# Kernel tuning notes

Hardware: AMD Instinct MI355X
Metric: run time of the kernel (lower is better)

The kernel has to match this reference:

```python
import jax, jax.numpy as jnp
import numpy as np

N, CIO, L = 16, 512, 384
DIMHEAD, NUMHEAD, MAXEMBED, DIMGROUP = 64, 8, 384, 8
CHID = DIMHEAD * NUMHEAD


def setup_inputs() -> dict:
    key = jax.random.key(0)
    ks = jax.random.split(key, 12)
    s = 0.05
    return {
        "x": jax.random.normal(ks[0], (N, CIO, L), jnp.float32),
        "xorg": jax.random.normal(ks[1], (N, CIO, L), jnp.float32),
        "abspos": jax.random.normal(ks[2], (N, CIO, L), jnp.float32),
        "mask": jnp.zeros((N, L), jnp.float32),
        "norm": jnp.full((N,), 8.0, jnp.float32),
        "qkpos_res": s * jax.random.normal(ks[3], (CIO // DIMGROUP, 1), jnp.float32),
        "qkorg_res": s * jax.random.normal(ks[4], (CIO // DIMGROUP, 1), jnp.float32),
        "vorg_res": s * jax.random.normal(ks[5], (CIO // DIMGROUP, 1), jnp.float32),
        "relpos": s * jax.random.normal(ks[6], (2 * MAXEMBED - 1,), jnp.float32),
        "gate_w": s * jax.random.normal(ks[7], (NUMHEAD, CIO), jnp.float32),
        "gate_b": jnp.zeros((NUMHEAD,), jnp.float32),
        "q_w": s * jax.random.normal(ks[8], (CHID, CIO), jnp.float32),
        "k_w": s * jax.random.normal(ks[9], (CHID, CIO), jnp.float32),
        "v_w": s * jax.random.normal(ks[10], (CHID, CIO), jnp.float32),
        "dense_w": s * jax.random.normal(ks[11], (CIO, CHID), jnp.float32),
        "dense_b": jnp.zeros((CIO,), jnp.float32),
    }


def _rezero(t, res):
    # (N,C,L) -> reshape to (N, C//DIMGROUP, DIMGROUP*L), scale per group, reshape back
    n, c, l = t.shape
    return (t.reshape(n, c // DIMGROUP, -1) * res).reshape(n, c, l)


def _relpos_idx():
    # idx[i, j] = clip(MAXEMBED - i + j, 0, 2*MAXEMBED - 2)
    idx = np.arange(MAXEMBED, MAXEMBED - L, -1)[:, None] + np.arange(L)[None, :]
    return jnp.asarray(np.clip(idx, 0, 2 * MAXEMBED - 2))


def reference(x, xorg, abspos, mask, norm, qkpos_res, qkorg_res, vorg_res,
              relpos, gate_w, gate_b, q_w, k_w, v_w, dense_w, dense_b):
    n = x.shape[0]
    x0 = x + _rezero(xorg, vorg_res)                     # value path
    x1 = x + _rezero(xorg, qkorg_res) + _rezero(abspos, qkpos_res)  # qk path

    q = jnp.einsum('oc,ncl->nol', q_w, x1).reshape(n, NUMHEAD, DIMHEAD, L)
    k = jnp.einsum('oc,ncl->nol', k_w, x1).reshape(n, NUMHEAD, DIMHEAD, L)
    v = jnp.einsum('oc,ncl->nol', v_w, x0).reshape(n, NUMHEAD, DIMHEAD, L)

    scores = jnp.einsum('nhdi,nhdj->nhij', q, k)         # (N, H, L, L)
    gate = jnp.einsum('oc,ncl->nol', gate_w, x) + gate_b[None, :, None]  # (N, H, L)
    scores = (scores + relpos[_relpos_idx()]
              + gate[:, :, None, :]
              + mask[:, None, None, :]) / norm[:, None, None, None]

    attn = jax.nn.softmax(scores, axis=-1)
    out = jnp.einsum('nhij,nhdj->nhdi', attn, v).reshape(n, CHID, L)
    out = jnp.einsum('oc,ncl->nol', dense_w, out) + dense_b[None, :, None]
    return out
```

## Files before the change

### kernel.cpp

```cpp
#include <hip/hip_runtime.h>
#include <hip/hip_bf16.h>

#define N_B   16
#define CIO   512
#define LSEQ  384
#define DH    64
#define NH    8
#define CHID  512
#define ME    384

typedef __hip_bfloat16 bf16;
typedef __attribute__((ext_vector_type(8))) short bf16x8;
typedef __attribute__((ext_vector_type(4))) float f32x4;

#define AS1 __attribute__((address_space(1)))
#define AS3 __attribute__((address_space(3)))

__device__ __forceinline__ unsigned short f2bs(float f) {
    union { bf16 b; unsigned short u; } cv; cv.b = __float2bfloat16(f); return cv.u;
}

__device__ __forceinline__ void gload_lds16(const bf16* g, bf16* l) {
    __builtin_amdgcn_global_load_lds((const AS1 unsigned int*)g,
                                     (AS3 unsigned int*)l, 16, 0, 0);
}

__launch_bounds__(256)
__global__ void prep_kernel(const float* __restrict__ x, const float* __restrict__ xorg,
                            const float* __restrict__ abspos,
                            const float* __restrict__ qkorg, const float* __restrict__ qkpos,
                            const float* __restrict__ vorg,
                            const float* __restrict__ gw,
                            const float* __restrict__ q_w, const float* __restrict__ k_w,
                            const float* __restrict__ v_w, const float* __restrict__ dense_w,
                            bf16* __restrict__ wqb, bf16* __restrict__ wkb,
                            bf16* __restrict__ wvb, bf16* __restrict__ wdb,
                            bf16* __restrict__ x1t, bf16* __restrict__ x0t,
                            float* __restrict__ gpart)
{
    __shared__ bf16 T1[64 * 72], T0[64 * 72];
    __shared__ float Traw[64 * 65];
    __shared__ float gws[NH * 64];
    __shared__ float r0[64], r1[64], r2[64];
    const int tid = threadIdx.x;
    const int cb = blockIdx.x;
    const int c0 = cb * 64;
    const int l0 = blockIdx.y * 64;
    const int n  = blockIdx.z;

    {
        int f = blockIdx.x + 8 * (blockIdx.y + 6 * blockIdx.z);
        if (f < 512) {
            int e = (f * 256 + tid) * 8;
            int which = e >> 18;
            int off = e & ((1 << 18) - 1);
            const float* s = which == 0 ? q_w : which == 1 ? k_w : which == 2 ? v_w : dense_w;
            bf16* d       = which == 0 ? wqb : which == 1 ? wkb : which == 2 ? wvb : wdb;
            float4 f0 = *(const float4*)&s[off];
            float4 f1 = *(const float4*)&s[off + 4];
            unsigned short u[8] = {f2bs(f0.x), f2bs(f0.y), f2bs(f0.z), f2bs(f0.w),
                                   f2bs(f1.x), f2bs(f1.y), f2bs(f1.z), f2bs(f1.w)};
            *(uint4*)&d[off] = *(uint4*)u;
        }
    }

    if (tid < 64) {
        int gidx = (c0 + tid) >> 3;
        r0[tid] = vorg[gidx];
        r1[tid] = qkorg[gidx];
        r2[tid] = qkpos[gidx];
    }
    for (int t = tid; t < NH * 64; t += 256) {
        int h = t >> 6, c = t & 63;
        gws[t] = gw[h * CIO + c0 + c];
    }
    __syncthreads();
    const int l = tid & 63, cs = tid >> 6;
    #pragma unroll
    for (int r = 0; r < 16; r++) {
        int cl = r * 4 + cs;
        size_t gi = ((size_t)n * CIO + c0 + cl) * LSEQ + l0 + l;
        float xv = x[gi], xo = xorg[gi];
        Traw[cl * 65 + l] = xv;
        T0[l * 72 + cl] = __float2bfloat16(xv + r0[cl] * xo);
        T1[l * 72 + cl] = __float2bfloat16(xv + r1[cl] * xo + r2[cl] * abspos[gi]);
    }
    __syncthreads();
    for (int t = tid; t < NH * 64; t += 256) {
        int h = t >> 6, ll = t & 63;
        float s = 0.f;
        #pragma unroll
        for (int c = 0; c < 64; c++) s += gws[h * 64 + c] * Traw[c * 65 + ll];
        gpart[(((size_t)cb * N_B + n) * NH + h) * LSEQ + l0 + ll] = s;
    }
    #pragma unroll
    for (int t = 0; t < 2; t++) {
        int idx = t * 256 + tid;
        int lr = idx >> 3, u = idx & 7;
        size_t go = ((size_t)n * LSEQ + l0 + lr) * CIO + c0 + u * 8;
        *(uint4*)&x1t[go] = *(const uint4*)&T1[lr * 72 + u * 8];
        *(uint4*)&x0t[go] = *(const uint4*)&T0[lr * 72 + u * 8];
    }
}

__launch_bounds__(256)
__global__ void qkv_kernel(const bf16* __restrict__ wall,
                           const bf16* __restrict__ x1t, const bf16* __restrict__ x0t,
                           bf16* __restrict__ qb, bf16* __restrict__ kb,
                           bf16* __restrict__ vb)
{
    __shared__ __align__(16) char smem[32768];
    bf16* As = (bf16*)smem;
    bf16* Bs = (bf16*)(smem + 16384);
    bf16* S  = (bf16*)smem;

    const int tid = threadIdx.x;
    const int lane = tid & 63, w = tid >> 6;
    const int l15 = lane & 15, g = lane >> 4;
    const int Bid = blockIdx.x;
    const int rres = Bid & 7, qq = Bid >> 3;
    const int n = rres + 8 * (qq / 36);
    const int t = qq % 36;
    const int ot = t / 3;
    const int lt = t % 3;
    const int osub = (w & 1) * 64, lsub = (w >> 1) * 64;

    const bf16* Wt = wall + (size_t)(ot * 128) * CIO;
    const bf16* Bt = (ot < 8 ? x1t : x0t) + ((size_t)n * LSEQ + lt * 128) * CIO;

    int crow[4], ccol[4];
    #pragma unroll
    for (int j = 0; j < 4; j++) {
        int c = (w * 4 + j) * 64 + lane;
        crow[j] = c >> 3;
        ccol[j] = ((c & 7) ^ (crow[j] & 7)) * 8;
    }

    f32x4 acc[4][4];
    #pragma unroll
    for (int mt = 0; mt < 4; mt++)
        #pragma unroll
        for (int jt = 0; jt < 4; jt++) acc[mt][jt] = f32x4{0.f, 0.f, 0.f, 0.f};

    const int swl = (l15 & 7);

    for (int it = 0; it < 8; ++it) {
        const int k0 = it * 64;
        #pragma unroll
        for (int j = 0; j < 4; j++) {
            gload_lds16(Wt + (size_t)crow[j] * CIO + k0 + ccol[j], As + (w * 4 + j) * 512);
            gload_lds16(Bt + (size_t)crow[j] * CIO + k0 + ccol[j], Bs + (w * 4 + j) * 512);
        }
        __syncthreads();
        #pragma unroll
        for (int kk = 0; kk < 2; kk++) {
            const int cS = ((kk * 4 + g) ^ swl) * 8;
            bf16x8 af[4], bfv[4];
            #pragma unroll
            for (int mt = 0; mt < 4; mt++)
                af[mt] = *(const bf16x8*)&As[(osub + mt * 16 + l15) * 64 + cS];
            #pragma unroll
            for (int jt = 0; jt < 4; jt++)
                bfv[jt] = *(const bf16x8*)&Bs[(lsub + jt * 16 + l15) * 64 + cS];
            #pragma unroll
            for (int mt = 0; mt < 4; mt++)
                #pragma unroll
                for (int jt = 0; jt < 4; jt++)
                    acc[mt][jt] = __builtin_amdgcn_mfma_f32_16x16x32_bf16(af[mt], bfv[jt], acc[mt][jt], 0, 0, 0);
        }
        __syncthreads();
    }

    if (ot < 8) {
        bf16* dstb = (ot < 4) ? qb : kb;
        const int hbase = 2 * (ot & 3);
        #pragma unroll
        for (int lh = 0; lh < 2; ++lh) {
            if ((w >> 1) == lh) {
                #pragma unroll
                for (int mt = 0; mt < 4; mt++)
                    #pragma unroll
                    for (int jt = 0; jt < 4; jt++)
                        #pragma unroll
                        for (int r = 0; r < 4; r++)
                            S[(jt * 16 + l15) * 136 + osub + mt * 16 + 4 * g + r] =
                                __float2bfloat16(acc[mt][jt][r]);
            }
            __syncthreads();
            #pragma unroll
            for (int t2 = 0; t2 < 4; ++t2) {
                int idx = t2 * 256 + tid;
                int lr = idx >> 4, u = idx & 15;
                int ho = u >> 3, dc = u & 7;
                bf16* dst = dstb + (((size_t)n * NH + hbase + ho) * LSEQ
                                    + lt * 128 + lh * 64 + lr) * DH + dc * 8;
                *(uint4*)dst = *(const uint4*)&S[lr * 136 + u * 8];
            }
            __syncthreads();
        }
    } else {
        const int ob = (ot - 8) * 128;
        #pragma unroll
        for (int oh = 0; oh < 2; ++oh) {
            if ((w & 1) == oh) {
                #pragma unroll
                for (int mt = 0; mt < 4; mt++)
                    #pragma unroll
                    for (int jt = 0; jt < 4; jt++)
                        #pragma unroll
                        for (int r = 0; r < 4; r++)
                            S[(mt * 16 + 4 * g + r) * 136 + lsub + jt * 16 + l15] =
                                __float2bfloat16(acc[mt][jt][r]);
            }
            __syncthreads();
            #pragma unroll
            for (int t2 = 0; t2 < 4; ++t2) {
                int idx = t2 * 256 + tid;
                int orr = idx >> 4, u = idx & 15;
                bf16* dst = vb + ((size_t)(n * CHID + ob + oh * 64 + orr)) * LSEQ
                               + lt * 128 + u * 8;
                *(uint4*)dst = *(const uint4*)&S[orr * 136 + u * 8];
            }
            __syncthreads();
        }
    }
}

#define KVT 64
#define NT  (LSEQ / KVT)

__launch_bounds__(256, 3)
__global__ void attn_kernel(const bf16* __restrict__ qt,
                            const bf16* __restrict__ kt,
                            const bf16* __restrict__ v,
                            const float* __restrict__ gpart,
                            const float* __restrict__ gb,
                            const float* __restrict__ mask,
                            const float* __restrict__ norm,
                            const float* __restrict__ relpos,
                            bf16* __restrict__ ctxt)
{
    __shared__ __align__(16) bf16 Kb[2][KVT * DH];
    __shared__ __align__(16) bf16 Vb[2][KVT * DH];
    __shared__ __align__(16) bf16 P[4 * 16 * 64];
    __shared__ float relp_s[2 * ME - 1];
    __shared__ float radd_s[LSEQ];

    const int tid = threadIdx.x;
    const int Bid = blockIdx.x;
    const int rres = Bid & 7, qq = Bid >> 3;
    const int n = rres + 8 * (qq / 48);
    const int rem = qq % 48;
    const int h = rem / 6;
    const int i0 = (rem % 6) * 64;
    const int lane = tid & 63;
    const int w = tid >> 6;
    const int l15 = lane & 15, g = lane >> 4;
    const int m0 = w * 16;

    const size_t nh = (size_t)n * NH + h;
    const bf16* kt_g = kt + nh * LSEQ * DH;
    const bf16* vg   = v + ((size_t)n * CHID + h * DH) * LSEQ;

    {
        const float gbh = gb[h];
        for (int i = tid; i < LSEQ; i += 256) {
            float s = gbh + mask[(size_t)n * LSEQ + i];
            #pragma unroll
            for (int cb = 0; cb < 8; cb++)
                s += gpart[(((size_t)cb * N_B + n) * NH + h) * LSEQ + i];
            radd_s[i] = s;
        }
    }
    for (int i = tid; i < 2 * ME - 1; i += 256) relp_s[i] = relpos[i];

    const bf16* qrow = qt + (nh * LSEQ + i0 + m0 + l15) * DH;
    bf16x8 a0 = *(const bf16x8*)&qrow[8 * g];
    bf16x8 a1 = *(const bf16x8*)&qrow[8 * g + 32];
    const float inv_norm = 1.0f / norm[n];

    const int c0_ = (2 * w) * 64 + lane;
    const int c1_ = (2 * w + 1) * 64 + lane;
    const int kr0 = c0_ >> 3, kc0 = ((c0_ & 7) ^ (kr0 & 7)) * 8;
    const int kr1 = c1_ >> 3, kc1 = ((c1_ & 7) ^ (kr1 & 7)) * 8;
    const int koff0 = kr0 * DH + kc0, koff1 = kr1 * DH + kc1;
    const int voff0 = kr0 * LSEQ + kc0, voff1 = kr1 * LSEQ + kc1;

    gload_lds16(kt_g + koff0, &Kb[0][(2 * w) * 512]);
    gload_lds16(kt_g + koff1, &Kb[0][(2 * w + 1) * 512]);
    gload_lds16(vg + voff0, &Vb[0][(2 * w) * 512]);
    gload_lds16(vg + voff1, &Vb[0][(2 * w + 1) * 512]);
    __syncthreads();

    const int ib = i0 + m0 + 4 * g;
    bf16* Pw = P + w * 1024;

    f32x4 oacc[4];
    #pragma unroll
    for (int dn = 0; dn < 4; dn++) oacc[dn] = f32x4{0.f, 0.f, 0.f, 0.f};
    float m_r[4]  = {-1e30f, -1e30f, -1e30f, -1e30f};
    float lsum[4] = {0.f, 0.f, 0.f, 0.f};

    #pragma unroll 2
    for (int t = 0; t < NT; ++t) {
        const int cur = t & 1;
        if (t + 1 < NT) {
            const bf16* kn = kt_g + (t + 1) * (KVT * DH);
            const bf16* vn = vg + (t + 1) * KVT;
            gload_lds16(kn + koff0, &Kb[cur ^ 1][(2 * w) * 512]);
            gload_lds16(kn + koff1, &Kb[cur ^ 1][(2 * w + 1) * 512]);
            gload_lds16(vn + voff0, &Vb[cur ^ 1][(2 * w) * 512]);
            gload_lds16(vn + voff1, &Vb[cur ^ 1][(2 * w + 1) * 512]);
        }

        f32x4 acc[4];
        #pragma unroll
        for (int jt = 0; jt < 4; jt++) acc[jt] = f32x4{0.f, 0.f, 0.f, 0.f};
        #pragma unroll
        for (int jt = 0; jt < 4; jt++) {
            const int row = jt * 16 + l15;
            bf16x8 b0 = *(const bf16x8*)&Kb[cur][row * 64 + ((g ^ (row & 7)) * 8)];
            bf16x8 b1 = *(const bf16x8*)&Kb[cur][row * 64 + (((4 + g) ^ (row & 7)) * 8)];
            acc[jt] = __builtin_amdgcn_mfma_f32_16x16x32_bf16(a0, b0, acc[jt], 0, 0, 0);
            acc[jt] = __builtin_amdgcn_mfma_f32_16x16x32_bf16(a1, b1, acc[jt], 0, 0, 0);
        }

        float mx[4] = {-1e30f, -1e30f, -1e30f, -1e30f};
        #pragma unroll
        for (int jt = 0; jt < 4; jt++) {
            const int j = t * KVT + jt * 16 + l15;
            const float ra = radd_s[j];
            const int idxb = ME - ib + j;
            #pragma unroll
            for (int r = 0; r < 4; r++) {
                int idx = idxb - r;
                idx = (idx > 2 * ME - 2) ? (2 * ME - 2) : idx;
                float s = (acc[jt][r] + relp_s[idx] + ra) * inv_norm;
                acc[jt][r] = s;
                mx[r] = fmaxf(mx[r], s);
            }
        }
        #pragma unroll
        for (int r = 0; r < 4; r++) {
            #pragma unroll
            for (int off = 1; off <= 8; off <<= 1)
                mx[r] = fmaxf(mx[r], __shfl_xor(mx[r], off));
            float mnew = fmaxf(m_r[r], mx[r]);
            float sc = __expf(m_r[r] - mnew);
            m_r[r] = mnew;
            lsum[r] *= sc;
            #pragma unroll
            for (int dn = 0; dn < 4; dn++) oacc[dn][r] *= sc;
        }
        #pragma unroll
        for (int jt = 0; jt < 4; jt++) {
            const int col = jt * 16 + l15;
            #pragma unroll
            for (int r = 0; r < 4; r++) {
                const int lr = 4 * g + r;
                float e = __expf(acc[jt][r] - m_r[r]);
                lsum[r] += e;
                Pw[lr * 64 + (col ^ ((lr & 7) << 3))] = __float2bfloat16(e);
            }
        }

        #pragma unroll
        for (int kh = 0; kh < 2; kh++) {
            bf16x8 a = *(const bf16x8*)&Pw[l15 * 64 + (((kh * 4 + g) ^ (l15 & 7)) * 8)];
            #pragma unroll
            for (int dn = 0; dn < 4; dn++) {
                const int vr = dn * 16 + l15;
                bf16x8 bv = *(const bf16x8*)&Vb[cur][vr * 64 + (((kh * 4 + g) ^ (vr & 7)) * 8)];
                oacc[dn] = __builtin_amdgcn_mfma_f32_16x16x32_bf16(a, bv, oacc[dn], 0, 0, 0);
            }
        }
        __syncthreads();
    }

    float rs[4];
    #pragma unroll
    for (int r = 0; r < 4; r++) {
        float tm = lsum[r];
        #pragma unroll
        for (int off = 1; off <= 8; off <<= 1) tm += __shfl_xor(tm, off);
        rs[r] = 1.0f / tm;
    }

    bf16* O = &Kb[0][0];
    #pragma unroll
    for (int dn = 0; dn < 4; dn++)
        #pragma unroll
        for (int r = 0; r < 4; r++)
            O[(m0 + 4 * g + r) * 72 + dn * 16 + l15] = __float2bfloat16(oacc[dn][r] * rs[r]);
    __syncthreads();

    bf16* cg_ = ctxt + ((size_t)n * LSEQ + i0) * CHID + h * DH;
    #pragma unroll
    for (int t = 0; t < 2; t++) {
        int idx = t * 256 + tid;
        int ir = idx >> 3, u = idx & 7;
        *(uint4*)&cg_[(size_t)ir * CHID + u * 8] = *(const uint4*)&O[ir * 72 + u * 8];
    }
}

__launch_bounds__(256, 6)
__global__ void dense_kernel(const bf16* __restrict__ Wb,
                             const bf16* __restrict__ Bt,
                             const float* __restrict__ bias,
                             float* __restrict__ outf)
{
    __shared__ __align__(16) float S[64 * 68];
    const int tid = threadIdx.x;
    const int lane = tid & 63, w = tid >> 6;
    const int l15 = lane & 15, g = lane >> 4;
    const int Bid = blockIdx.x;
    const int rres = Bid & 7, qq = Bid >> 3;
    const int n = rres + 8 * (qq / 48);
    const int tt = qq % 48;
    const int o0 = (tt / 6) * 64;
    const int l0 = (tt % 6) * 64;

    const bf16* arow = Wb + (size_t)(o0 + l15) * CIO + 8 * g;
    const bf16* brow = Bt + ((size_t)n * LSEQ + l0 + w * 16 + l15) * CIO + 8 * g;

    f32x4 acc[4];
    #pragma unroll
    for (int mt = 0; mt < 4; mt++) acc[mt] = f32x4{0.f, 0.f, 0.f, 0.f};
    #pragma unroll 4
    for (int it = 0; it < 16; it++) {
        const int k0 = it * 32;
        bf16x8 b = *(const bf16x8*)&brow[k0];
        bf16x8 a[4];
        #pragma unroll
        for (int mt = 0; mt < 4; mt++)
            a[mt] = *(const bf16x8*)&arow[(size_t)mt * 16 * CIO + k0];
        #pragma unroll
        for (int mt = 0; mt < 4; mt++)
            acc[mt] = __builtin_amdgcn_mfma_f32_16x16x32_bf16(a[mt], b, acc[mt], 0, 0, 0);
    }

    #pragma unroll
    for (int mt = 0; mt < 4; mt++)
        #pragma unroll
        for (int r = 0; r < 4; r++)
            S[(mt * 16 + 4 * g + r) * 68 + w * 16 + l15] =
                acc[mt][r] + bias[o0 + mt * 16 + 4 * g + r];
    __syncthreads();
    float* og = outf + ((size_t)n * CHID + o0) * LSEQ + l0;
    #pragma unroll
    for (int t = 0; t < 4; t++) {
        int idx = t * 256 + tid;
        int orow = idx >> 4, u = idx & 15;
        *(float4*)&og[(size_t)orow * LSEQ + u * 4] = *(const float4*)&S[orow * 68 + u * 4];
    }
}

extern "C" void kernel_launch(void* const* d_in, const int* in_sizes, int n_in,
                              void* d_out, int out_size, void* d_ws, size_t ws_size,
                              hipStream_t stream)
{
    const float* x       = (const float*)d_in[0];
    const float* xorg    = (const float*)d_in[1];
    const float* abspos  = (const float*)d_in[2];
    const float* mask    = (const float*)d_in[3];
    const float* norm    = (const float*)d_in[4];
    const float* qkpos   = (const float*)d_in[5];
    const float* qkorg   = (const float*)d_in[6];
    const float* vorg    = (const float*)d_in[7];
    const float* relpos  = (const float*)d_in[8];
    const float* gate_w  = (const float*)d_in[9];
    const float* gate_b  = (const float*)d_in[10];
    const float* q_w     = (const float*)d_in[11];
    const float* k_w     = (const float*)d_in[12];
    const float* v_w     = (const float*)d_in[13];
    const float* dense_w = (const float*)d_in[14];
    const float* dense_b = (const float*)d_in[15];
    float* out = (float*)d_out;

    const size_t TEN = (size_t)N_B * CHID * LSEQ * sizeof(bf16);
    const size_t WB  = (size_t)CHID * CIO * sizeof(bf16);
    char* ws = (char*)d_ws;
    bf16*  x1t  = (bf16*)(ws);
    bf16*  x0t  = (bf16*)(ws + TEN);
    bf16*  qb   = (bf16*)(ws + 2 * TEN);
    bf16*  kb   = (bf16*)(ws + 3 * TEN);
    bf16*  vb   = (bf16*)(ws + 4 * TEN);
    bf16*  wqb  = (bf16*)(ws + 5 * TEN);
    bf16*  wkb  = (bf16*)(ws + 5 * TEN + WB);
    bf16*  wvb  = (bf16*)(ws + 5 * TEN + 2 * WB);
    bf16*  wdb  = (bf16*)(ws + 5 * TEN + 3 * WB);
    float* gpart = (float*)(ws + 5 * TEN + 4 * WB);
    bf16*  ctxt = x1t;

    prep_kernel<<<dim3(CIO / 64, LSEQ / 64, N_B), 256, 0, stream>>>(
        x, xorg, abspos, qkorg, qkpos, vorg, gate_w,
        q_w, k_w, v_w, dense_w, wqb, wkb, wvb, wdb, x1t, x0t, gpart);
    qkv_kernel<<<576, 256, 0, stream>>>(wqb, x1t, x0t, qb, kb, vb);
    attn_kernel<<<768, 256, 0, stream>>>(qb, kb, vb, gpart, gate_b,
                                         mask, norm, relpos, ctxt);
    dense_kernel<<<768, 256, 0, stream>>>(wdb, ctxt, dense_b, out);
}
```

Before: 179.0 us.

## Retile dense GEMM to 128x128 LDS-staged tiles with swizzled async loads

Restructures the output projection GEMM from 64x64 tiles that read operands directly from global memory into 128x128 tiles per block. Operands are staged in XOR-swizzled LDS through global_load_lds, and each wave computes a 64x64 sub-tile with 4x4 MFMAs. This increases operand reuse and cuts redundant global traffic. The trade-offs are fewer blocks (192, under one wave on the GPU), no double buffering, and a serialized four-pass epilogue through shared memory.

```diff
diff --git a/kernel.cpp b/kernel.cpp
--- a/kernel.cpp
+++ b/kernel.cpp
@@ -403,55 +403,99 @@
     }
 }
 
-__launch_bounds__(256, 6)
+__launch_bounds__(256)
 __global__ void dense_kernel(const bf16* __restrict__ Wb,
                              const bf16* __restrict__ Bt,
                              const float* __restrict__ bias,
                              float* __restrict__ outf)
 {
-    __shared__ __align__(16) float S[64 * 68];
+    __shared__ __align__(16) char smem[32768];
+    bf16* As = (bf16*)smem;
+    bf16* Bs = (bf16*)(smem + 16384);
+    float* Sf = (float*)smem;
+
     const int tid = threadIdx.x;
     const int lane = tid & 63, w = tid >> 6;
     const int l15 = lane & 15, g = lane >> 4;
     const int Bid = blockIdx.x;
     const int rres = Bid & 7, qq = Bid >> 3;
-    const int n = rres + 8 * (qq / 48);
-    const int tt = qq % 48;
-    const int o0 = (tt / 6) * 64;
-    const int l0 = (tt % 6) * 64;
-
-    const bf16* arow = Wb + (size_t)(o0 + l15) * CIO + 8 * g;
-    const bf16* brow = Bt + ((size_t)n * LSEQ + l0 + w * 16 + l15) * CIO + 8 * g;
-
-    f32x4 acc[4];
-    #pragma unroll
-    for (int mt = 0; mt < 4; mt++) acc[mt] = f32x4{0.f, 0.f, 0.f, 0.f};
-    #pragma unroll 4
-    for (int it = 0; it < 16; it++) {
-        const int k0 = it * 32;
-        bf16x8 b = *(const bf16x8*)&brow[k0];
-        bf16x8 a[4];
-        #pragma unroll
-        for (int mt = 0; mt < 4; mt++)
-            a[mt] = *(const bf16x8*)&arow[(size_t)mt * 16 * CIO + k0];
-        #pragma unroll
-        for (int mt = 0; mt < 4; mt++)
-            acc[mt] = __builtin_amdgcn_mfma_f32_16x16x32_bf16(a[mt], b, acc[mt], 0, 0, 0);
-    }
-
+    const int n = rres + 8 * (qq / 12);
+    const int t = qq % 12;
+    const int ot = t / 3;
+    const int lt = t % 3;
+    const int o0 = ot * 128, l0 = lt * 128;
+    const int osub = (w & 1) * 64, lsub = (w >> 1) * 64;
+
+    const bf16* Wt = Wb + (size_t)o0 * CIO;
+    const bf16* Btb = Bt + ((size_t)n * LSEQ + l0) * CIO;
+
+    int crow[4], ccol[4];
+    #pragma unroll
+    for (int j = 0; j < 4; j++) {
+        int c = (w * 4 + j) * 64 + lane;
+        crow[j] = c >> 3;
+        ccol[j] = ((c & 7) ^ (crow[j] & 7)) * 8;
+    }
+
+    f32x4 acc[4][4];
     #pragma unroll
     for (int mt = 0; mt < 4; mt++)
         #pragma unroll
-        for (int r = 0; r < 4; r++)
-            S[(mt * 16 + 4 * g + r) * 68 + w * 16 + l15] =
-                acc[mt][r] + bias[o0 + mt * 16 + 4 * g + r];
-    __syncthreads();
-    float* og = outf + ((size_t)n * CHID + o0) * LSEQ + l0;
-    #pragma unroll
-    for (int t = 0; t < 4; t++) {
-        int idx = t * 256 + tid;
-        int orow = idx >> 4, u = idx & 15;
-        *(float4*)&og[(size_t)orow * LSEQ + u * 4] = *(const float4*)&S[orow * 68 + u * 4];
+        for (int jt = 0; jt < 4; jt++) acc[mt][jt] = f32x4{0.f, 0.f, 0.f, 0.f};
+
+    const int swl = (l15 & 7);
+
+    for (int it = 0; it < 8; ++it) {
+        const int k0 = it * 64;
+        #pragma unroll
+        for (int j = 0; j < 4; j++) {
+            gload_lds16(Wt + (size_t)crow[j] * CIO + k0 + ccol[j], As + (w * 4 + j) * 512);
+            gload_lds16(Btb + (size_t)crow[j] * CIO + k0 + ccol[j], Bs + (w * 4 + j) * 512);
+        }
+        __syncthreads();
+        #pragma unroll
+        for (int kk = 0; kk < 2; kk++) {
+            const int cS = ((kk * 4 + g) ^ swl) * 8;
+            bf16x8 af[4], bfv[4];
+            #pragma unroll
+            for (int mt = 0; mt < 4; mt++)
+                af[mt] = *(const bf16x8*)&As[(osub + mt * 16 + l15) * 64 + cS];
+            #pragma unroll
+            for (int jt = 0; jt < 4; jt++)
+                bfv[jt] = *(const bf16x8*)&Bs[(lsub + jt * 16 + l15) * 64 + cS];
+            #pragma unroll
+            for (int mt = 0; mt < 4; mt++)
+                #pragma unroll
+                for (int jt = 0; jt < 4; jt++)
+                    acc[mt][jt] = __builtin_amdgcn_mfma_f32_16x16x32_bf16(af[mt], bfv[jt], acc[mt][jt], 0, 0, 0);
+        }
+        __syncthreads();
+    }
+
+    #pragma unroll
+    for (int p = 0; p < 4; ++p) {
+        const int oh = p & 1, lh = p >> 1;
+        if (w == p) {
+            #pragma unroll
+            for (int mt = 0; mt < 4; mt++) {
+                #pragma unroll
+                for (int r = 0; r < 4; r++) {
+                    const float bv = bias[o0 + osub + mt * 16 + 4 * g + r];
+                    #pragma unroll
+                    for (int jt = 0; jt < 4; jt++)
+                        Sf[(mt * 16 + 4 * g + r) * 68 + jt * 16 + l15] = acc[mt][jt][r] + bv;
+                }
+            }
+        }
+        __syncthreads();
+        float* og = outf + ((size_t)n * CHID + o0 + oh * 64) * LSEQ + l0 + lh * 64;
+        #pragma unroll
+        for (int t2 = 0; t2 < 4; ++t2) {
+            int idx = t2 * 256 + tid;
+            int orow = idx >> 4, u = idx & 15;
+            *(float4*)&og[(size_t)orow * LSEQ + u * 4] = *(const float4*)&Sf[orow * 68 + u * 4];
+        }
+        __syncthreads();
     }
 }
 
@@ -498,5 +542,5 @@
     qkv_kernel<<<576, 256, 0, stream>>>(wqb, x1t, x0t, qb, kb, vb);
     attn_kernel<<<768, 256, 0, stream>>>(qb, kb, vb, gpart, gate_b,
                                          mask, norm, relpos, ctxt);
-    dense_kernel<<<768, 256, 0, stream>>>(wdb, ctxt, dense_b, out);
-}
+    dense_kernel<<<192, 256, 0, stream>>>(wdb, ctxt, dense_b, out);
+}
```

Measured after the change: 161.6 us (median of 2 runs). 1.11x faster.
